# Kernel tuning notes

Hardware: AMD Instinct MI355X
Metric: run time of the kernel (lower is better)

## Reference

```python
import jax, jax.numpy as jnp
import numpy as np
import math

_DENSE_LOCAL_W = 64
_DYADIC = [96, 128, 192, 256, 384, 512, 768, 1024, 1536]
OFFSETS = sorted(set(range(0, _DENSE_LOCAL_W + 1)) | set(_DYADIC))  # 74 offsets

B, N, D, H = 1, 2048, 1024, 16
HD = D // H


def setup_inputs() -> dict:
    key = jax.random.key(0)
    ks = jax.random.split(key, 8)
    s = 1.0 / math.sqrt(D)
    x = jax.random.normal(ks[0], (B, N, D), dtype=jnp.float32)
    Wqkv = jax.random.uniform(ks[1], (3 * D, D), jnp.float32, -s, s)
    bqkv = jax.random.uniform(ks[2], (3 * D,), jnp.float32, -s, s)
    Wgate = jax.random.uniform(ks[3], (D, D), jnp.float32, -s, s)
    bgate = jax.random.uniform(ks[4], (D,), jnp.float32, -s, s)
    Wout = jax.random.uniform(ks[5], (D, D), jnp.float32, -s, s)
    bout = jax.random.uniform(ks[6], (D,), jnp.float32, -s, s)
    # pos_bias init exactly as in the module: -log(1+delta) * alpha_h, shape (O, H)
    alphas = jnp.linspace(0.2, 2.0, H)
    deltas = jnp.array([math.log(1.0 + d) for d in OFFSETS], dtype=jnp.float32)
    pos_bias = -deltas[:, None] * alphas[None, :]
    offsets = jnp.array(OFFSETS, dtype=jnp.int32)
    return {"x": x, "Wqkv": Wqkv, "bqkv": bqkv, "Wgate": Wgate, "bgate": bgate,
            "Wout": Wout, "bout": bout, "pos_bias": pos_bias, "offsets": offsets}


def reference(x, Wqkv, bqkv, Wgate, bgate, Wout, bout, pos_bias, offsets):
    Bx, Nx, Dx = x.shape
    qkv = x @ Wqkv.T + bqkv                       # (B, N, 3D)
    q, k, v = jnp.split(qkv, 3, axis=-1)
    q = q.reshape(Bx, Nx, H, HD).transpose(0, 2, 1, 3)  # (B, H, N, HD)
    k = k.reshape(Bx, Nx, H, HD).transpose(0, 2, 1, 3)
    v = v.reshape(Bx, Nx, H, HD).transpose(0, 2, 1, 3)
    scale = HD ** -0.5

    # gather shifted K/V: position n attends to n - delta for each fixed offset
    n_idx = jnp.arange(Nx, dtype=jnp.int32)[:, None]      # (N, 1)
    idx = n_idx - offsets[None, :]                        # (N, O)
    valid = idx >= 0                                      # (N, O)
    idx_c = jnp.clip(idx, 0, Nx - 1)
    K_all = k[:, :, idx_c, :]                             # (B, H, N, O, HD)
    V_all = v[:, :, idx_c, :]

    scores = jnp.einsum('bhnd,bhnod->bhno', q, K_all) * scale
    scores = scores + pos_bias.T[None, :, None, :]        # (1, H, 1, O)
    scores = jnp.where(valid[None, None], scores, -jnp.inf)
    alpha = jax.nn.softmax(scores, axis=-1)               # (B, H, N, O)
    out = jnp.einsum('bhno,bhnod->bhnd', alpha, V_all)    # (B, H, N, HD)

    flat = out.transpose(0, 2, 1, 3).reshape(Bx, Nx, Dx)  # (B, N, D)
    gate = jax.nn.sigmoid(x @ Wgate.T + bgate)
    return (flat * gate) @ Wout.T + bout                  # dropout = identity (eval)
```

## Files before the change

### kernel.cpp

```cpp
#include <hip/hip_runtime.h>
#include <hip/hip_bf16.h>

#define SEQ_N 2048
#define DIM   1024
#define NHEAD 16
#define HDIM  64
#define LDQ   4096
#define NOFF  74
#define NDENSE 65
#define NJ    224
#define NT    16
#define PST   232
#define QST   88

typedef __attribute__((ext_vector_type(8)))  __bf16 bv8;
typedef __attribute__((ext_vector_type(4)))  __bf16 bv4;
typedef __attribute__((ext_vector_type(4)))  float  f32x4;
typedef __attribute__((ext_vector_type(16))) float  f32x16;

typedef __attribute__((address_space(3))) void as3_void;
typedef __attribute__((address_space(1))) void as1_void;

__device__ __forceinline__ void async16(const void* g, void* l) {
  __builtin_amdgcn_global_load_lds((as1_void*)(unsigned long long)g,
                                   (as3_void*)l, 16, 0, 0);
}

#define E1 (SEQ_N * DIM)
#define E2 (E1 + 3 * DIM * DIM)
#define E3 (E2 + DIM * DIM)
#define E4 (E3 + DIM * DIM)
__global__ __launch_bounds__(256) void cvt_all(
    const float* __restrict__ x, const float* __restrict__ wqkv,
    const float* __restrict__ wgate, const float* __restrict__ wout,
    __bf16* __restrict__ dst) {
  long i = ((long)blockIdx.x * 256 + threadIdx.x) * 4;
  if (i >= E4) return;
  const float* s; long o;
  if (i < E1)      { s = x;     o = i; }
  else if (i < E2) { s = wqkv;  o = i - E1; }
  else if (i < E3) { s = wgate; o = i - E2; }
  else             { s = wout;  o = i - E3; }
  float4 v = *(const float4*)(s + o);
  bv4 ov;
  ov[0] = (__bf16)v.x; ov[1] = (__bf16)v.y; ov[2] = (__bf16)v.z; ov[3] = (__bf16)v.w;
  *(bv4*)(dst + i) = ov;
}

#define BM 128
#define BKT 128

template <int BN_, typename OutT>
__global__ __launch_bounds__(256) void gemm_bt(
    const __bf16* __restrict__ A, const __bf16* __restrict__ B1,
    const __bf16* __restrict__ B2, const float* __restrict__ bias1,
    const float* __restrict__ bias2, int Nsplit,
    OutT* __restrict__ C, int ldc, int K) {
  __shared__ __attribute__((aligned(16))) __bf16 Asm[BM * BKT];
  __shared__ __attribute__((aligned(16))) __bf16 Bsm[BN_ * BKT];
  constexpr int NJ32 = BN_ / 64;
  constexpr int CA = BM * BKT / 8;
  constexpr int CB = BN_ * BKT / 8;
  constexpr int CPR = BKT / 8;

  const int tid  = threadIdx.x;
  const int lane = tid & 63;
  const int wave = tid >> 6;
  const int wr = wave >> 1, wc = wave & 1;
  const int m31 = lane & 31;
  const int h1  = lane >> 5;
  const int l7  = lane & 7;

  const int bn0 = blockIdx.x * BN_;
  const int bm0 = blockIdx.y * BM;

  const __bf16* Bp;
  const float* biasp;
  if (bn0 < Nsplit) { Bp = B1 + (size_t)bn0 * K;            biasp = bias1 + bn0; }
  else              { Bp = B2 + (size_t)(bn0 - Nsplit) * K; biasp = bias2 + (bn0 - Nsplit); }
  const __bf16* Ap = A + (size_t)bm0 * K;

  f32x16 acc[2][NJ32] = {};

  for (int kt = 0; kt < K; kt += BKT) {
    __syncthreads();
#pragma unroll
    for (int c0 = 0; c0 < CA + CB; c0 += 256) {
      int c = c0 + tid;
      if (c < CA) {
        int rr = c / CPR, qq = c % CPR;
        int qs = qq ^ (rr & 7);
        async16(Ap + (size_t)rr * K + kt + qs * 8, Asm + c * 8);
      } else {
        int cb = c - CA;
        int rr = cb / CPR, qq = cb % CPR;
        int qs = qq ^ (rr & 7);
        async16(Bp + (size_t)rr * K + kt + qs * 8, Bsm + cb * 8);
      }
    }
    __syncthreads();

#pragma unroll
    for (int kk = 0; kk < BKT / 16; ++kk) {
      const int qs = ((kk * 2 + h1) ^ l7) * 8;
      bv8 af[2], bfr[NJ32];
#pragma unroll
      for (int i = 0; i < 2; ++i)
        af[i] = *(const bv8*)(Asm + (wr * 64 + i * 32 + m31) * BKT + qs);
#pragma unroll
      for (int j = 0; j < NJ32; ++j)
        bfr[j] = *(const bv8*)(Bsm + (wc * (BN_ / 2) + j * 32 + m31) * BKT + qs);
#pragma unroll
      for (int i = 0; i < 2; ++i)
#pragma unroll
        for (int j = 0; j < NJ32; ++j)
          acc[i][j] = __builtin_amdgcn_mfma_f32_32x32x16_bf16(af[i], bfr[j], acc[i][j], 0, 0, 0);
    }
  }

#pragma unroll
  for (int i = 0; i < 2; ++i) {
#pragma unroll
    for (int j = 0; j < NJ32; ++j) {
      int ccol = wc * (BN_ / 2) + j * 32 + m31;
      float b = biasp[ccol];
#pragma unroll
      for (int reg = 0; reg < 16; ++reg) {
        int row = bm0 + wr * 64 + i * 32 + (reg & 3) + 8 * (reg >> 2) + 4 * h1;
        C[(size_t)row * ldc + bn0 + ccol] = (OutT)(acc[i][j][reg] + b);
      }
    }
  }
}

template <typename OutT>
__global__ __launch_bounds__(256) void gemm_bt64(
    const __bf16* __restrict__ A, const __bf16* __restrict__ B,
    const float* __restrict__ bias, OutT* __restrict__ C, int ldc, int K) {
  __shared__ __attribute__((aligned(16))) __bf16 Asm[64 * BKT];
  __shared__ __attribute__((aligned(16))) __bf16 Bsm[64 * BKT];
  constexpr int CM = 64 * BKT / 8;
  constexpr int CPR = BKT / 8;

  const int tid  = threadIdx.x;
  const int lane = tid & 63;
  const int wave = tid >> 6;
  const int wr = wave >> 1, wc = wave & 1;
  const int m31 = lane & 31;
  const int h1  = lane >> 5;
  const int l7  = lane & 7;

  const int bn0 = blockIdx.x * 64;
  const int bm0 = blockIdx.y * 64;

  const __bf16* Ap = A + (size_t)bm0 * K;
  const __bf16* Bp = B + (size_t)bn0 * K;
  const float* biasp = bias + bn0;

  f32x16 acc = {};

  for (int kt = 0; kt < K; kt += BKT) {
    __syncthreads();
#pragma unroll
    for (int c0 = 0; c0 < CM; c0 += 256) {
      int c = c0 + tid;
      int rr = c / CPR, qq = c % CPR;
      int qs = qq ^ (rr & 7);
      async16(Ap + (size_t)rr * K + kt + qs * 8, Asm + c * 8);
      async16(Bp + (size_t)rr * K + kt + qs * 8, Bsm + c * 8);
    }
    __syncthreads();

#pragma unroll
    for (int kk = 0; kk < BKT / 16; ++kk) {
      const int qs = ((kk * 2 + h1) ^ l7) * 8;
      bv8 a = *(const bv8*)(Asm + (wr * 32 + m31) * BKT + qs);
      bv8 b = *(const bv8*)(Bsm + (wc * 32 + m31) * BKT + qs);
      acc = __builtin_amdgcn_mfma_f32_32x32x16_bf16(a, b, acc, 0, 0, 0);
    }
  }

  {
    int ccol = wc * 32 + m31;
    float b = biasp[ccol];
#pragma unroll
    for (int reg = 0; reg < 16; ++reg) {
      int row = bm0 + wr * 32 + (reg & 3) + 8 * (reg >> 2) + 4 * h1;
      C[(size_t)row * ldc + bn0 + ccol] = (OutT)(acc[reg] + b);
    }
  }
}

__global__ __launch_bounds__(256) void attn_mfma(
    const __bf16* __restrict__ qkv,
    const float* __restrict__ pos_bias,
    const int* __restrict__ offsets,
    __bf16* __restrict__ fg) {
  const int n0 = (blockIdx.x >> 4) * NT;
  const int h  = blockIdx.x & 15;
  const int tid = threadIdx.x;
  const int lane = tid & 63;
  const int w = tid >> 6;
  const int fr = lane & 15, fq = lane >> 4;
  const int fr7 = fr & 7;

  __shared__ __attribute__((aligned(16))) __bf16 KVbuf[NJ * HDIM];
  __shared__ __attribute__((aligned(16))) __bf16 Qbuf[NT * QST];
  __shared__ __attribute__((aligned(16))) float  Sbuf[NT][80];
  __shared__ __attribute__((aligned(16))) __bf16 Pd[NT * PST];
  __shared__ float inv_l[NT];

  const int ch = lane & 7;
  const int rowin = lane >> 3;

  if (tid < 128) {
    int ni = tid >> 3, cq = tid & 7;
    bv8 q = *(const bv8*)(qkv + (size_t)(n0 + ni) * LDQ + h * HDIM + cq * 8);
    *(bv8*)(Qbuf + ni * QST + cq * 8) = q;
  }
#pragma unroll
  for (int c0 = 0; c0 < NT * PST / 8; c0 += 256) {
    int c = c0 + tid;
    if (c < NT * PST / 8) *(uint4*)(Pd + c * 8) = make_uint4(0, 0, 0, 0);
  }
  {
    int chs = ch ^ rowin;
#pragma unroll
    for (int it = 0; it < 7; ++it) {
      int jbase = it * 32 + w * 8;
      int j = jbase + rowin;
      int g;
      if (j < 80) g = n0 - 64 + j;
      else { int jj = j - 80; g = n0 - offsets[NDENSE + (jj >> 4)] + (jj & 15); }
      if (g < 0) g = 0;
      async16(qkv + (size_t)g * LDQ + DIM + h * HDIM + chs * 8,
              KVbuf + jbase * HDIM + lane * 8);
    }
  }
  __syncthreads();

  for (int jb = w; jb < 14; jb += 4) {
    f32x4 acc = {};
#pragma unroll
    for (int kk = 0; kk < 2; ++kk) {
      bv8 a = *(const bv8*)(Qbuf + fr * QST + kk * 32 + fq * 8);
      bv8 b = *(const bv8*)(KVbuf + (jb * 16 + fr) * HDIM + ((kk * 4 + fq) ^ fr7) * 8);
      acc = __builtin_amdgcn_mfma_f32_16x16x32_bf16(a, b, acc, 0, 0, 0);
    }
    int j = jb * 16 + fr;
    if (jb < 5) {
      bool gvalid = (n0 - 64 + j) >= 0;
#pragma unroll
      for (int r = 0; r < 4; ++r) {
        int ni = fq * 4 + r;
        int o = ni + 64 - j;
        if (o >= 0 && o < NDENSE)
          Sbuf[ni][o] = gvalid ? acc[r] : -3.0e38f;
      }
    } else {
      int jj = j - 80;
      int s = jj >> 4, tni = jj & 15;
      int r = tni - fq * 4;
      if (r >= 0 && r < 4) {
        bool gvalid = (n0 + tni - offsets[NDENSE + s]) >= 0;
        Sbuf[tni][NDENSE + s] = gvalid ? acc[r] : -3.0e38f;
      }
    }
  }
  __syncthreads();

#pragma unroll
  for (int it = 0; it < 7; ++it) {
    int jbase = it * 32 + w * 8;
    int j = jbase + rowin;
    int g;
    if (j < 80) g = n0 - 64 + j;
    else { int jj = j - 80; g = n0 - offsets[NDENSE + (jj >> 4)] + (jj & 15); }
    if (g < 0) g = 0;
    async16(qkv + (size_t)g * LDQ + 2 * DIM + h * HDIM + ch * 8,
            KVbuf + jbase * HDIM + lane * 8);
  }

  {
    int t = tid & 15, ni = tid >> 4;
    float sc5[5];
    float m = -3.0e38f;
#pragma unroll
    for (int k = 0; k < 5; ++k) {
      int o = t + k * 16;
      float v = -3.0e38f;
      if (o < NOFF) {
        float raw = Sbuf[ni][o];
        if (raw > -1.0e38f) v = raw * 0.125f + pos_bias[o * NHEAD + h];
      }
      sc5[k] = v;
      m = fmaxf(m, v);
    }
#pragma unroll
    for (int d = 1; d < 16; d <<= 1) m = fmaxf(m, __shfl_xor(m, d));
    float sum = 0.f;
#pragma unroll
    for (int k = 0; k < 5; ++k) {
      int o = t + k * 16;
      if (o < NOFF && sc5[k] > -1.0e38f) {
        float e = __expf(sc5[k] - m);
        sum += e;
        int j = (o < NDENSE) ? (ni + 64 - o) : (80 + (o - NDENSE) * 16 + ni);
        Pd[ni * PST + j] = (__bf16)e;
      }
    }
#pragma unroll
    for (int d = 1; d < 16; d <<= 1) sum += __shfl_xor(sum, d);
    if (t == 0) inv_l[ni] = 1.f / sum;
  }
  __syncthreads();

  {
    const int db = w;
    f32x4 acc = {};
#pragma unroll
    for (int kt = 0; kt < 7; ++kt) {
      bv8 a = *(const bv8*)(Pd + fr * PST + kt * 32 + fq * 8);
      bv8 b;
#pragma unroll
      for (int jj = 0; jj < 8; ++jj)
        b[jj] = KVbuf[(kt * 32 + fq * 8 + jj) * HDIM + db * 16 + fr];
      acc = __builtin_amdgcn_mfma_f32_16x16x32_bf16(a, b, acc, 0, 0, 0);
    }
    int d = db * 16 + fr;
#pragma unroll
    for (int r = 0; r < 4; ++r) {
      int ni = fq * 4 + r;
      float o = acc[r] * inv_l[ni];
      float gp = (float)qkv[(size_t)(n0 + ni) * LDQ + 3 * DIM + h * HDIM + d];
      float gate = 1.f / (1.f + __expf(-gp));
      fg[(size_t)(n0 + ni) * DIM + h * HDIM + d] = (__bf16)(o * gate);
    }
  }
}

extern "C" void kernel_launch(void* const* d_in, const int* in_sizes, int n_in,
                              void* d_out, int out_size, void* d_ws, size_t ws_size,
                              hipStream_t stream) {
  const float* x        = (const float*)d_in[0];
  const float* Wqkv     = (const float*)d_in[1];
  const float* bqkv     = (const float*)d_in[2];
  const float* Wgate    = (const float*)d_in[3];
  const float* bgate    = (const float*)d_in[4];
  const float* Wout     = (const float*)d_in[5];
  const float* bout     = (const float*)d_in[6];
  const float* pos_bias = (const float*)d_in[7];
  const int*   offsets  = (const int*)d_in[8];
  float* out = (float*)d_out;

  __bf16* xb       = (__bf16*)d_ws;
  __bf16* Wqkvb    = xb    + (size_t)SEQ_N * DIM;
  __bf16* Wgateb   = Wqkvb + (size_t)3 * DIM * DIM;
  __bf16* Woutb    = Wgateb + (size_t)DIM * DIM;
  __bf16* qkvg     = Woutb + (size_t)DIM * DIM;
  __bf16* flatgate = qkvg + (size_t)SEQ_N * LDQ;

  cvt_all<<<dim3(E4 / 1024), dim3(256), 0, stream>>>(x, Wqkv, Wgate, Wout, xb);

  gemm_bt<128, __bf16><<<dim3(LDQ / 128, SEQ_N / BM), dim3(256), 0, stream>>>(
      xb, Wqkvb, Wgateb, bqkv, bgate, 3 * DIM, qkvg, LDQ, DIM);

  attn_mfma<<<dim3((SEQ_N / NT) * NHEAD), dim3(256), 0, stream>>>(
      qkvg, pos_bias, offsets, flatgate);

  gemm_bt64<float><<<dim3(DIM / 64, SEQ_N / 64), dim3(256), 0, stream>>>(
      flatgate, Woutb, bout, out, DIM, DIM);
}
```

Before: 140.8 us.

## Assign GEMM tiles per XCC via atomic counters for L2 locality

Both GEMM kernels now claim tiles dynamically through per-XCC atomic counters read via the XCC_ID hardware register. Each XCC takes a contiguous 8x8 block of output tiles, so its blocks share A and B panels in that die's L2. The counters are zeroed inside the conversion kernel, and blocks spill over to other regions when their own region is exhausted. The cost is an atomic plus a barrier at every block start and a dependency on counter state in the workspace.

```diff
diff --git a/kernel.cpp b/kernel.cpp
--- a/kernel.cpp
+++ b/kernel.cpp
@@ -26,6 +26,22 @@
                                    (as3_void*)l, 16, 0, 0);
 }
 
+__device__ __forceinline__ int claim_tile(int* cnt) {
+  int xcc;
+  asm volatile("s_getreg_b32 %0, hwreg(HW_REG_XCC_ID)" : "=s"(xcc));
+  int r = xcc & 7;
+  int t = atomicAdd(&cnt[r], 1);
+  if (t >= 64) {
+#pragma unroll
+    for (int k = 1; k < 8; ++k) {
+      int r2 = (r + k) & 7;
+      t = atomicAdd(&cnt[r2], 1);
+      if (t < 64) { r = r2; break; }
+    }
+  }
+  return (r << 6) | (t & 63);
+}
+
 #define E1 (SEQ_N * DIM)
 #define E2 (E1 + 3 * DIM * DIM)
 #define E3 (E2 + DIM * DIM)
@@ -33,7 +49,8 @@
 __global__ __launch_bounds__(256) void cvt_all(
     const float* __restrict__ x, const float* __restrict__ wqkv,
     const float* __restrict__ wgate, const float* __restrict__ wout,
-    __bf16* __restrict__ dst) {
+    __bf16* __restrict__ dst, int* __restrict__ cnt) {
+  if (blockIdx.x == 0 && threadIdx.x < 16) cnt[threadIdx.x] = 0;
   long i = ((long)blockIdx.x * 256 + threadIdx.x) * 4;
   if (i >= E4) return;
   const float* s; long o;
@@ -55,9 +72,10 @@
     const __bf16* __restrict__ A, const __bf16* __restrict__ B1,
     const __bf16* __restrict__ B2, const float* __restrict__ bias1,
     const float* __restrict__ bias2, int Nsplit,
-    OutT* __restrict__ C, int ldc, int K) {
+    OutT* __restrict__ C, int ldc, int K, int* __restrict__ cnt) {
   __shared__ __attribute__((aligned(16))) __bf16 Asm[BM * BKT];
   __shared__ __attribute__((aligned(16))) __bf16 Bsm[BN_ * BKT];
+  __shared__ int s_tile;
   constexpr int NJ32 = BN_ / 64;
   constexpr int CA = BM * BKT / 8;
   constexpr int CB = BN_ * BKT / 8;
@@ -71,8 +89,12 @@
   const int h1  = lane >> 5;
   const int l7  = lane & 7;
 
-  const int bn0 = blockIdx.x * BN_;
-  const int bm0 = blockIdx.y * BM;
+  if (tid == 0) s_tile = claim_tile(cnt);
+  __syncthreads();
+  const int tle = s_tile;
+  const int rg = tle >> 6, tt = tle & 63;
+  const int bn0 = (((rg & 3) << 3) + (tt & 7)) * BN_;
+  const int bm0 = (((rg >> 2) << 3) + (tt >> 3)) * BM;
 
   const __bf16* Bp;
   const float* biasp;
@@ -136,9 +158,11 @@
 template <typename OutT>
 __global__ __launch_bounds__(256) void gemm_bt64(
     const __bf16* __restrict__ A, const __bf16* __restrict__ B,
-    const float* __restrict__ bias, OutT* __restrict__ C, int ldc, int K) {
+    const float* __restrict__ bias, OutT* __restrict__ C, int ldc, int K,
+    int* __restrict__ cnt) {
   __shared__ __attribute__((aligned(16))) __bf16 Asm[64 * BKT];
   __shared__ __attribute__((aligned(16))) __bf16 Bsm[64 * BKT];
+  __shared__ int s_tile;
   constexpr int CM = 64 * BKT / 8;
   constexpr int CPR = BKT / 8;
 
@@ -150,8 +174,12 @@
   const int h1  = lane >> 5;
   const int l7  = lane & 7;
 
-  const int bn0 = blockIdx.x * 64;
-  const int bm0 = blockIdx.y * 64;
+  if (tid == 0) s_tile = claim_tile(cnt);
+  __syncthreads();
+  const int tle = s_tile;
+  const int rg = tle >> 6, tt = tle & 63;
+  const int bn0 = (((rg & 1) << 3) + (tt & 7)) * 64;
+  const int bm0 = (((rg >> 1) << 3) + (tt >> 3)) * 64;
 
   const __bf16* Ap = A + (size_t)bm0 * K;
   const __bf16* Bp = B + (size_t)bn0 * K;
@@ -359,15 +387,16 @@
   __bf16* Woutb    = Wgateb + (size_t)DIM * DIM;
   __bf16* qkvg     = Woutb + (size_t)DIM * DIM;
   __bf16* flatgate = qkvg + (size_t)SEQ_N * LDQ;
-
-  cvt_all<<<dim3(E4 / 1024), dim3(256), 0, stream>>>(x, Wqkv, Wgate, Wout, xb);
-
-  gemm_bt<128, __bf16><<<dim3(LDQ / 128, SEQ_N / BM), dim3(256), 0, stream>>>(
-      xb, Wqkvb, Wgateb, bqkv, bgate, 3 * DIM, qkvg, LDQ, DIM);
+  int*    cnt      = (int*)(flatgate + (size_t)SEQ_N * DIM);
+
+  cvt_all<<<dim3(E4 / 1024), dim3(256), 0, stream>>>(x, Wqkv, Wgate, Wout, xb, cnt);
+
+  gemm_bt<128, __bf16><<<dim3(512), dim3(256), 0, stream>>>(
+      xb, Wqkvb, Wgateb, bqkv, bgate, 3 * DIM, qkvg, LDQ, DIM, cnt);
 
   attn_mfma<<<dim3((SEQ_N / NT) * NHEAD), dim3(256), 0, stream>>>(
       qkvg, pos_bias, offsets, flatgate);
 
-  gemm_bt64<float><<<dim3(DIM / 64, SEQ_N / 64), dim3(256), 0, stream>>>(
-      flatgate, Woutb, bout, out, DIM, DIM);
-}
+  gemm_bt64<float><<<dim3(512), dim3(256), 0, stream>>>(
+      flatgate, Woutb, bout, out, DIM, DIM, cnt + 8);
+}
```

New measurement: 151.8 us. 1.08x slower.
